# Optimization experiments

Measured on AMD Instinct MI355X. Metric: run time of the kernel, lower is better.

The kernel has to match this reference:

```python
import jax, jax.numpy as jnp
import numpy as np

B, IN, COND, H, LAT, E, GH = 8192, 256, 1024, 1024, 128, 6, 64
INP = LAT + COND      # decoder layer0 input size = 1152
INTER = LAT + H       # decoder layer1/2 input size = 1152


def setup_inputs() -> dict:
    key = jax.random.key(0)
    ks = jax.random.split(key, 30)
    n = lambda k, shape, s=0.02: jax.random.normal(k, shape, dtype=jnp.float32) * s
    return {
        'x': jax.random.normal(ks[0], (B, IN), dtype=jnp.float32),
        'y': jax.random.normal(ks[1], (B, COND), dtype=jnp.float32),
        'eps': jax.random.normal(ks[2], (B, LAT), dtype=jnp.float32),
        # encoder: layer k input = prev_dim + IN (x is re-concatenated each layer)
        'enc_w0': n(ks[3], (IN + COND + IN, H)), 'enc_b0': jnp.zeros((H,), jnp.float32),
        'enc_w1': n(ks[4], (H + IN, H)),         'enc_b1': jnp.zeros((H,), jnp.float32),
        'mu_w': n(ks[5], (H, LAT)),  'mu_b': jnp.zeros((LAT,), jnp.float32),
        'lv_w': n(ks[6], (H, LAT)),  'lv_b': jnp.zeros((LAT,), jnp.float32),
        # gating network (input = latent + cond)
        'g_w0': n(ks[7], (INP, GH)), 'g_b0': jnp.zeros((GH,), jnp.float32),
        'g_w1': n(ks[8], (GH, GH)),  'g_b1': jnp.zeros((GH,), jnp.float32),
        'g_w2': n(ks[9], (GH, E)),   'g_b2': jnp.zeros((E,), jnp.float32),
        # expert weights [E, in, out] and biases [E, out] (bias init 0.01 as in source)
        'exp_w0': n(ks[10], (E, INP, H)),   'exp_b0': jnp.full((E, H), 0.01, jnp.float32),
        'exp_w1': n(ks[11], (E, INTER, H)), 'exp_b1': jnp.full((E, H), 0.01, jnp.float32),
        'exp_w2': n(ks[12], (E, INTER, IN)), 'exp_b2': jnp.full((E, IN), 0.01, jnp.float32),
    }


def _forward(x, y, eps, enc_w0, enc_b0, enc_w1, enc_b1, mu_w, mu_b, lv_w, lv_b,
             g_w0, g_b0, g_w1, g_b1, g_w2, g_b2,
             exp_w0, exp_b0, exp_w1, exp_b1, exp_w2, exp_b2):
    elu = jax.nn.elu
    # --- Encoder ---
    h = jnp.concatenate([x, y], axis=1)
    h = elu(jnp.concatenate([h, x], axis=1) @ enc_w0 + enc_b0)
    h = elu(jnp.concatenate([h, x], axis=1) @ enc_w1 + enc_b1)
    mu = h @ mu_w + mu_b
    logvar = h @ lv_w + lv_b
    # --- Reparameterize (eps passed explicitly for determinism) ---
    z = mu + eps * jnp.exp(0.5 * logvar)
    # --- MixedDecoder ---
    g = jnp.concatenate([z, y], axis=1)
    g = elu(g @ g_w0 + g_b0)
    g = elu(g @ g_w1 + g_b1)
    coeff = jax.nn.softmax(g @ g_w2 + g_b2, axis=1)  # [B, E]
    layer_out = y
    for W, bb, act in ((exp_w0, exp_b0, True), (exp_w1, exp_b1, True), (exp_w2, exp_b2, False)):
        inp = jnp.concatenate([z, layer_out], axis=1)  # [B, I]
        # fused mixture-of-experts projection: avoids materializing per-sample [B,I,O] weight
        out = coeff @ bb + jnp.einsum('be,bi,eio->bo', coeff, inp, W)
        layer_out = elu(out) if act else out
    return layer_out, mu, logvar


def reference(x, y, eps, enc_w0, enc_b0, enc_w1, enc_b1, mu_w, mu_b, lv_w, lv_b,
              g_w0, g_b0, g_w1, g_b1, g_w2, g_b2,
              exp_w0, exp_b0, exp_w1, exp_b1, exp_w2, exp_b2):
    return _forward(x, y, eps, enc_w0, enc_b0, enc_w1, enc_b1, mu_w, mu_b, lv_w, lv_b,
                    g_w0, g_b0, g_w1, g_b1, g_w2, g_b2,
                    exp_w0, exp_b0, exp_w1, exp_b1, exp_w2, exp_b2)
```

## Files before the change

kernel.cpp:

```cpp
#include <hip/hip_runtime.h>
#include <hip/hip_bf16.h>
#include <cstddef>

using u16 = unsigned short;
using short8 = __attribute__((ext_vector_type(8))) short;
using f32x4 = __attribute__((ext_vector_type(4))) float;

constexpr int B_   = 8192;
constexpr int IN_  = 256;
constexpr int COND_= 1024;
constexpr int H_   = 1024;
constexpr int LAT_ = 128;
constexpr int NE_  = 6;
constexpr int GH_  = 64;
constexpr int INP_ = 1152;
constexpr int K0_  = 1536;
constexpr int K1_  = 1280;

constexpr int BK = 64;

typedef const __attribute__((address_space(1))) void gv_t;
typedef __attribute__((address_space(3))) void lv_t;
#define GLDS(g, l) __builtin_amdgcn_global_load_lds((gv_t*)(g), (lv_t*)(l), 16, 0, 0)

__device__ __forceinline__ u16 f2b(float f) {
  __hip_bfloat16 h = __float2bfloat16(f);
  return *reinterpret_cast<u16*>(&h);
}
__device__ __forceinline__ float elu1(float x) { return x > 0.f ? x : (__expf(x) - 1.f); }

__global__ void k_transpose(const float* __restrict__ in, u16* __restrict__ out,
                            int R, int C, long inStride, long outStride) {
  __shared__ float t[32][33];
  const float* ip = in + (long)blockIdx.z * inStride;
  u16* op = out + (long)blockIdx.z * outStride;
  int c0 = blockIdx.x * 32, r0 = blockIdx.y * 32;
  int tx = threadIdx.x, ty = threadIdx.y;
#pragma unroll
  for (int i = 0; i < 4; i++) {
    int r = r0 + ty + i * 8, c = c0 + tx;
    if (r < R && c < C) t[ty + i * 8][tx] = ip[(long)r * C + c];
  }
  __syncthreads();
#pragma unroll
  for (int i = 0; i < 4; i++) {
    int c = c0 + ty + i * 8, r = r0 + tx;
    if (r < R && c < C) op[(long)c * R + r] = f2b(t[tx][ty + i * 8]);
  }
}

__global__ void k_prep(const float* __restrict__ x, const float* __restrict__ y,
                       u16* __restrict__ A0, u16* __restrict__ A1) {
  long idx = (long)blockIdx.x * blockDim.x + threadIdx.x;
  long n0 = (long)B_ * K0_;
  if (idx < n0) {
    int b = (int)(idx / K0_), c = (int)(idx % K0_);
    float v;
    if (c < IN_)            v = x[(long)b * IN_ + c];
    else if (c < IN_+COND_) v = y[(long)b * COND_ + (c - IN_)];
    else                    v = x[(long)b * IN_ + (c - IN_ - COND_)];
    A0[idx] = f2b(v);
  } else {
    long j = idx - n0;
    if (j < (long)B_ * IN_) {
      int b = (int)(j / IN_), c = (int)(j % IN_);
      A1[(long)b * K1_ + H_ + c] = f2b(x[(long)b * IN_ + c]);
    }
  }
}

__global__ void k_z(const float* __restrict__ mu, const float* __restrict__ lv,
                    const float* __restrict__ eps, const float* __restrict__ y,
                    u16* __restrict__ ZY, u16* __restrict__ D1, u16* __restrict__ D2) {
  long idx = (long)blockIdx.x * blockDim.x + threadIdx.x;
  if (idx >= (long)B_ * INP_) return;
  int b = (int)(idx / INP_), c = (int)(idx % INP_);
  if (c < LAT_) {
    long o = (long)b * LAT_ + c;
    float z = mu[o] + eps[o] * __expf(0.5f * lv[o]);
    u16 zb = f2b(z);
    ZY[idx] = zb; D1[idx] = zb; D2[idx] = zb;
  } else {
    ZY[idx] = f2b(y[(long)b * COND_ + (c - LAT_)]);
  }
}

__global__ __launch_bounds__(256) void k_gate(const float* __restrict__ G1,
    const float* __restrict__ w1, const float* __restrict__ b1,
    const float* __restrict__ w2, const float* __restrict__ b2,
    float* __restrict__ coeff) {
  __shared__ float W1[64][65];
  __shared__ float W2[64][8];
  __shared__ float B1[64], B2[8];
  int tid = threadIdx.x;
  for (int i = tid; i < 64 * 64; i += 256) W1[i >> 6][i & 63] = w1[i];
  for (int i = tid; i < 64 * 6; i += 256) W2[i / 6][i % 6] = w2[i];
  if (tid < 64) B1[tid] = b1[tid];
  if (tid < 8)  B2[tid] = (tid < 6) ? b2[tid] : 0.f;
  __syncthreads();
  int row = blockIdx.x * 256 + tid;
  const float* gr = G1 + (long)row * GH_;
  float g[64];
#pragma unroll
  for (int i = 0; i < 16; i++) {
    float4 v = *(const float4*)(gr + i * 4);
    g[i*4] = v.x; g[i*4+1] = v.y; g[i*4+2] = v.z; g[i*4+3] = v.w;
  }
  float lg[6];
#pragma unroll
  for (int e = 0; e < 6; e++) lg[e] = B2[e];
  for (int n = 0; n < 64; n++) {
    float s = B1[n];
#pragma unroll
    for (int k = 0; k < 64; k++) s += g[k] * W1[k][n];
    s = elu1(s);
#pragma unroll
    for (int e = 0; e < 6; e++) lg[e] += s * W2[n][e];
  }
  float m = lg[0];
#pragma unroll
  for (int e = 1; e < 6; e++) m = fmaxf(m, lg[e]);
  float p[6], sum = 0.f;
#pragma unroll
  for (int e = 0; e < 6; e++) { p[e] = __expf(lg[e] - m); sum += p[e]; }
  float inv = 1.f / sum;
#pragma unroll
  for (int e = 0; e < 6; e++) coeff[(long)row * 6 + e] = p[e] * inv;
}

template<int MREP, bool MOE>
__global__ __launch_bounds__(256, 2) void k_gemm(
    const u16* __restrict__ A, int lda,
    const u16* __restrict__ WT, long wstride,
    const float* __restrict__ bias,
    const float* __restrict__ coeff,
    int N, int K, int E,
    u16* __restrict__ outH, float* __restrict__ outF, float* __restrict__ outF2,
    int ldo, int splitcol, const float* __restrict__ bias2, int act)
{
  constexpr int BMt = 32 * MREP;
  __shared__ __align__(16) u16 As[2][BMt][BK];
  __shared__ __align__(16) u16 Bs[2][128][BK];
  __shared__ float Cf[MOE ? BMt : 1][8];

  const int tid = threadIdx.x;
  const int lane = tid & 63, w = tid >> 6;
  const int wr = w >> 1, wc = w & 1;
  const int brow = blockIdx.x * BMt, bcol = blockIdx.y * 128;
  const int lr = lane & 15, hi = lane >> 4;
  const int lk = hi * 8;
  const int xsw = (lr & 7) << 3;

  if (MOE && tid < BMt) {
#pragma unroll
    for (int e2 = 0; e2 < 8; e2++)
      Cf[tid][e2] = (e2 < 6) ? coeff[(long)(brow + tid) * 6 + e2] : 0.f;
  }

  f32x4 acc[MREP][4];
#pragma unroll
  for (int m = 0; m < MREP; m++)
#pragma unroll
    for (int n = 0; n < 4; n++)
#pragma unroll
      for (int r = 0; r < 4; r++) acc[m][n][r] = 0.f;

  const int srow = w * 8 + (lane >> 3);
  const int sdst = (lane & 7) * 8;
  const int ssrc = ((lane & 7) ^ ((lane >> 3) & 7)) * 8;
  const u16* Asrc = A + (long)(brow + srow) * lda + ssrc;
  const u16* Bsrc = WT + (long)(bcol + srow) * K + ssrc;
  const int KSTEPS = K / BK;

  int cur = 0;
#pragma unroll
  for (int i = 0; i < BMt / 32; i++)
    GLDS(Asrc + (long)(i * 32) * lda, &As[0][i * 32 + srow][sdst]);
#pragma unroll
  for (int i = 0; i < 4; i++)
    GLDS(Bsrc + (long)(i * 32) * K, &Bs[0][i * 32 + srow][sdst]);

  for (int e = 0; e < E; ++e) {
    f32x4 pacc[MREP][4];
    if constexpr (MOE) {
#pragma unroll
      for (int m = 0; m < MREP; m++)
#pragma unroll
        for (int n = 0; n < 4; n++)
#pragma unroll
          for (int r = 0; r < 4; r++) pacc[m][n][r] = 0.f;
    }

    for (int kt = 0; kt < KSTEPS; ++kt) {
      __syncthreads();
      int ne = e, nk = kt + 1;
      if (nk == KSTEPS) { nk = 0; ne = e + 1; }
      if (ne < E) {
        const u16* ap = Asrc + (long)nk * BK;
        const u16* bp = Bsrc + (long)ne * wstride + (long)nk * BK;
#pragma unroll
        for (int i = 0; i < BMt / 32; i++)
          GLDS(ap + (long)(i * 32) * lda, &As[cur ^ 1][i * 32 + srow][sdst]);
#pragma unroll
        for (int i = 0; i < 4; i++)
          GLDS(bp + (long)(i * 32) * K, &Bs[cur ^ 1][i * 32 + srow][sdst]);
      }
#pragma unroll
      for (int kk = 0; kk < BK; kk += 32) {
        short8 af[MREP], bfr[4];
        const int cc = (kk + lk) ^ xsw;
#pragma unroll
        for (int m = 0; m < MREP; m++)
          af[m] = *(const short8*)&As[cur][wr * (16 * MREP) + m * 16 + lr][cc];
#pragma unroll
        for (int n = 0; n < 4; n++)
          bfr[n] = *(const short8*)&Bs[cur][wc * 64 + n * 16 + lr][cc];
#pragma unroll
        for (int m = 0; m < MREP; m++)
#pragma unroll
          for (int n = 0; n < 4; n++) {
            if constexpr (MOE)
              pacc[m][n] = __builtin_amdgcn_mfma_f32_16x16x32_bf16(af[m], bfr[n], pacc[m][n], 0, 0, 0);
            else
              acc[m][n] = __builtin_amdgcn_mfma_f32_16x16x32_bf16(af[m], bfr[n], acc[m][n], 0, 0, 0);
          }
      }
      cur ^= 1;
    }
    if constexpr (MOE) {
#pragma unroll
      for (int m = 0; m < MREP; m++)
#pragma unroll
        for (int r = 0; r < 4; r++) {
          float c = Cf[wr * (16 * MREP) + m * 16 + hi * 4 + r][e];
#pragma unroll
          for (int n = 0; n < 4; n++) acc[m][n][r] += c * pacc[m][n][r];
        }
    }
  }

#pragma unroll
  for (int m = 0; m < MREP; m++)
#pragma unroll
    for (int n = 0; n < 4; n++) {
      int col = bcol + wc * 64 + n * 16 + lr;
      if (col >= N) continue;
#pragma unroll
      for (int r = 0; r < 4; r++) {
        int rowl = wr * (16 * MREP) + m * 16 + hi * 4 + r;
        long row = brow + rowl;
        float v = acc[m][n][r];
        if constexpr (MOE) {
          float bv = 0.f;
#pragma unroll
          for (int e = 0; e < 6; e++) bv += Cf[rowl][e] * bias[(long)e * N + col];
          v += bv;
        } else {
          v += (col < splitcol) ? bias[col] : bias2[col - splitcol];
        }
        if (act) v = elu1(v);
        if (outH) outH[row * ldo + col] = f2b(v);
        else if (col < splitcol) outF[row * ldo + col] = v;
        else outF2[row * ldo + (col - splitcol)] = v;
      }
    }
}

extern "C" void kernel_launch(void* const* d_in, const int* in_sizes, int n_in,
                              void* d_out, int out_size, void* d_ws, size_t ws_size,
                              hipStream_t stream) {
  (void)in_sizes; (void)out_size;
  if (n_in < 23) return;
  const float* x      = (const float*)d_in[0];
  const float* y      = (const float*)d_in[1];
  const float* eps    = (const float*)d_in[2];
  const float* enc_w0 = (const float*)d_in[3];
  const float* enc_b0 = (const float*)d_in[4];
  const float* enc_w1 = (const float*)d_in[5];
  const float* enc_b1 = (const float*)d_in[6];
  const float* mu_w   = (const float*)d_in[7];
  const float* mu_b   = (const float*)d_in[8];
  const float* lv_w   = (const float*)d_in[9];
  const float* lv_b   = (const float*)d_in[10];
  const float* g_w0   = (const float*)d_in[11];
  const float* g_b0   = (const float*)d_in[12];
  const float* g_w1   = (const float*)d_in[13];
  const float* g_b1   = (const float*)d_in[14];
  const float* g_w2   = (const float*)d_in[15];
  const float* g_b2   = (const float*)d_in[16];
  const float* exp_w0 = (const float*)d_in[17];
  const float* exp_b0 = (const float*)d_in[18];
  const float* exp_w1 = (const float*)d_in[19];
  const float* exp_b1 = (const float*)d_in[20];
  const float* exp_w2 = (const float*)d_in[21];
  const float* exp_b2 = (const float*)d_in[22];

  char* ws = (char*)d_ws;
  size_t off = 0;
  auto alloc = [&](size_t bytes) -> void* {
    void* p = ws + off; off += (bytes + 255) & ~(size_t)255; return p;
  };
  u16* A0     = (u16*)alloc((size_t)B_ * K0_ * 2);
  u16* A1     = (u16*)alloc((size_t)B_ * K1_ * 2);
  u16* H2     = (u16*)alloc((size_t)B_ * H_ * 2);
  u16* ZY     = (u16*)alloc((size_t)B_ * INP_ * 2);
  u16* encw0T = (u16*)alloc((size_t)K0_ * H_ * 2);
  u16* encw1T = (u16*)alloc((size_t)K1_ * H_ * 2);
  u16* mulvT  = (u16*)alloc((size_t)256 * H_ * 2);
  u16* gw0T   = (u16*)alloc((size_t)GH_ * INP_ * 2);
  u16* ew0T   = (u16*)alloc((size_t)NE_ * H_ * INP_ * 2);
  if (ws_size < off) return;

  u16* D1 = A0;
  u16* D2 = A1;
  float* G1    = (float*)H2;
  float* COEFF = (float*)((char*)H2 + (size_t)B_ * GH_ * 4);
  u16* ew2T = (u16*)((char*)H2 + (size_t)4 * 1024 * 1024);
  u16* ew1T = ZY;

  float* outO = (float*)d_out;
  float* muO  = outO + (size_t)B_ * IN_;
  float* lvO  = muO + (size_t)B_ * LAT_;

  dim3 tb(32, 8);
  k_transpose<<<dim3(32, 48), tb, 0, stream>>>(enc_w0, encw0T, K0_, H_, 0, 0);
  k_transpose<<<dim3(32, 40), tb, 0, stream>>>(enc_w1, encw1T, K1_, H_, 0, 0);
  k_transpose<<<dim3(4, 32),  tb, 0, stream>>>(mu_w, mulvT, H_, LAT_, 0, 0);
  k_transpose<<<dim3(4, 32),  tb, 0, stream>>>(lv_w, mulvT + (size_t)LAT_ * H_, H_, LAT_, 0, 0);
  k_transpose<<<dim3(2, 36),  tb, 0, stream>>>(g_w0, gw0T, INP_, GH_, 0, 0);
  k_transpose<<<dim3(32, 36, NE_), tb, 0, stream>>>(exp_w0, ew0T, INP_, H_,
                                                    (long)INP_ * H_, (long)INP_ * H_);
  long npr = (long)B_ * K0_ + (long)B_ * IN_;
  k_prep<<<(int)((npr + 255) / 256), 256, 0, stream>>>(x, y, A0, A1);

  k_gemm<4, false><<<dim3(B_ / 128, H_ / 128), 256, 0, stream>>>(A0, K0_, encw0T, 0, enc_b0,
      nullptr, H_, K0_, 1, A1, nullptr, nullptr, K1_, H_, nullptr, 1);
  k_gemm<4, false><<<dim3(B_ / 128, H_ / 128), 256, 0, stream>>>(A1, K1_, encw1T, 0, enc_b1,
      nullptr, H_, K1_, 1, H2, nullptr, nullptr, H_, H_, nullptr, 1);
  k_gemm<2, false><<<dim3(B_ / 64, 2), 256, 0, stream>>>(H2, H_, mulvT, 0, mu_b, nullptr,
      256, H_, 1, nullptr, muO, lvO, LAT_, LAT_, lv_b, 0);

  k_transpose<<<dim3(8, 36, NE_), tb, 0, stream>>>(exp_w2, ew2T, INP_, IN_,
                                                   (long)INP_ * IN_, (long)INP_ * IN_);
  long nz = (long)B_ * INP_;
  k_z<<<(int)((nz + 255) / 256), 256, 0, stream>>>(muO, lvO, eps, y, ZY, D1, D2);

  k_gemm<2, false><<<dim3(B_ / 64, 1), 256, 0, stream>>>(ZY, INP_, gw0T, 0, g_b0, nullptr,
      GH_, INP_, 1, nullptr, G1, nullptr, GH_, GH_, nullptr, 1);
  k_gate<<<B_ / 256, 256, 0, stream>>>(G1, g_w1, g_b1, g_w2, g_b2, COEFF);

  k_gemm<4, true><<<dim3(B_ / 128, H_ / 128), 256, 0, stream>>>(ZY, INP_, ew0T, (long)H_ * INP_,
      exp_b0, COEFF, H_, INP_, NE_, D1 + LAT_, nullptr, nullptr, INP_, H_, nullptr, 1);
  k_transpose<<<dim3(32, 36, NE_), tb, 0, stream>>>(exp_w1, ew1T, INP_, H_,
                                                    (long)INP_ * H_, (long)INP_ * H_);
  k_gemm<4, true><<<dim3(B_ / 128, H_ / 128), 256, 0, stream>>>(D1, INP_, ew1T, (long)H_ * INP_,
      exp_b1, COEFF, H_, INP_, NE_, D2 + LAT_, nullptr, nullptr, INP_, H_, nullptr, 1);
  k_gemm<2, true><<<dim3(B_ / 64, 2), 256, 0, stream>>>(D2, INP_, ew2T, (long)IN_ * INP_,
      exp_b2, COEFF, IN_, INP_, NE_, nullptr, outO, nullptr, IN_, IN_, nullptr, 0);
}
```

Before: 599.1 us.

## Add 256x128-tile triple-buffered GEMM kernel for encoder and MoE expert layers

Introduces k_gemm8, a 512-thread kernel with 256x128 output tiles, a three-stage LDS buffer fed by global_load_lds with explicit vmcnt waits, XOR-swizzled LDS layout, and a block-index remap so blocks that share columns run close together. Both encoder GEMMs and the two large expert GEMMs now use it. The aim is more data reuse per tile and deeper overlap of loads with MFMA work. In exchange it uses more LDS and registers per block, which may lower occupancy.

```diff
diff --git a/kernel.cpp b/kernel.cpp
--- a/kernel.cpp
+++ b/kernel.cpp
@@ -126,6 +126,154 @@
   float inv = 1.f / sum;
 #pragma unroll
   for (int e = 0; e < 6; e++) coeff[(long)row * 6 + e] = p[e] * inv;
+}
+
+template<int KSTEPS, int E, bool MOE>
+__global__ __launch_bounds__(512, 2) void k_gemm8(
+    const u16* __restrict__ A,
+    const u16* __restrict__ WT,
+    const float* __restrict__ bias,
+    const float* __restrict__ coeff,
+    int N,
+    u16* __restrict__ outH, int ldo)
+{
+  constexpr int KK = KSTEPS * BK;
+  constexpr int T = E * KSTEPS;
+  __shared__ __align__(16) u16 As[3][256][BK];
+  __shared__ __align__(16) u16 Bs[3][128][BK];
+  __shared__ float Cf[MOE ? 256 : 1][8];
+
+  const int tid = threadIdx.x;
+  const int lane = tid & 63, w = tid >> 6;
+  const int wr = w >> 1, wc = w & 1;
+  const int lin = blockIdx.x + blockIdx.y * gridDim.x;
+  const int sl = (lin & 7) * 32 + (lin >> 3);
+  const int brow = (sl & 31) * 256, bcol = (sl >> 5) * 128;
+  const int lr = lane & 15, hi = lane >> 4;
+  const int lk = hi * 8;
+  const int xsw = (lr & 7) << 3;
+
+  if (MOE) {
+    if (tid < 256) {
+#pragma unroll
+      for (int e2 = 0; e2 < 8; e2++)
+        Cf[tid][e2] = (e2 < 6) ? coeff[(long)(brow + tid) * 6 + e2] : 0.f;
+    }
+    __syncthreads();
+  }
+
+  f32x4 acc[4][4];
+#pragma unroll
+  for (int m = 0; m < 4; m++)
+#pragma unroll
+    for (int n = 0; n < 4; n++)
+#pragma unroll
+      for (int r = 0; r < 4; r++) acc[m][n][r] = 0.f;
+  f32x4 pacc[MOE ? 4 : 1][MOE ? 4 : 1];
+  if constexpr (MOE) {
+#pragma unroll
+    for (int m = 0; m < 4; m++)
+#pragma unroll
+      for (int n = 0; n < 4; n++)
+#pragma unroll
+        for (int r = 0; r < 4; r++) pacc[m][n][r] = 0.f;
+  }
+
+  const int srow = w * 8 + (lane >> 3);
+  const int sdst = (lane & 7) * 8;
+  const int ssrc = ((lane & 7) ^ ((lane >> 3) & 7)) * 8;
+  const u16* Asrc = A + (long)(brow + srow) * KK + ssrc;
+  const u16* Bsrc = WT + (long)(bcol + srow) * KK + ssrc;
+
+  auto STAGE = [&](int t2, int buf) {
+    const int e2 = (E == 1) ? 0 : (t2 / KSTEPS);
+    const int k2 = (E == 1) ? t2 : (t2 % KSTEPS);
+    const u16* ap = Asrc + k2 * BK;
+    const u16* bp = Bsrc + (long)e2 * ((long)N * KK) + k2 * BK;
+#pragma unroll
+    for (int i = 0; i < 4; i++)
+      GLDS(ap + (long)(i * 64) * KK, &As[buf][i * 64 + srow][sdst]);
+#pragma unroll
+    for (int i = 0; i < 2; i++)
+      GLDS(bp + (long)(i * 64) * KK, &Bs[buf][i * 64 + srow][sdst]);
+  };
+
+  STAGE(0, 0);
+  STAGE(1, 1);
+
+  for (int t = 0; t < T; ++t) {
+    if (t + 1 < T) asm volatile("s_waitcnt vmcnt(6)" ::: "memory");
+    else           asm volatile("s_waitcnt vmcnt(0)" ::: "memory");
+    asm volatile("s_barrier" ::: "memory");
+    if (t + 2 < T) STAGE(t + 2, (t + 2) % 3);
+    const int cur = t % 3;
+#pragma unroll
+    for (int kk = 0; kk < BK; kk += 32) {
+      short8 af[4], bfr[4];
+      const int cc = (kk + lk) ^ xsw;
+#pragma unroll
+      for (int m = 0; m < 4; m++)
+        af[m] = *(const short8*)&As[cur][wr * 64 + m * 16 + lr][cc];
+#pragma unroll
+      for (int n = 0; n < 4; n++)
+        bfr[n] = *(const short8*)&Bs[cur][wc * 64 + n * 16 + lr][cc];
+      __builtin_amdgcn_s_setprio(1);
+#pragma unroll
+      for (int m = 0; m < 4; m++)
+#pragma unroll
+        for (int n = 0; n < 4; n++) {
+          if constexpr (MOE)
+            pacc[m][n] = __builtin_amdgcn_mfma_f32_16x16x32_bf16(af[m], bfr[n], pacc[m][n], 0, 0, 0);
+          else
+            acc[m][n] = __builtin_amdgcn_mfma_f32_16x16x32_bf16(af[m], bfr[n], acc[m][n], 0, 0, 0);
+        }
+      __builtin_amdgcn_s_setprio(0);
+    }
+    if constexpr (MOE) {
+      if ((t + 1) % KSTEPS == 0) {
+        const int e = t / KSTEPS;
+#pragma unroll
+        for (int m = 0; m < 4; m++)
+#pragma unroll
+          for (int r = 0; r < 4; r++) {
+            float c = Cf[wr * 64 + m * 16 + hi * 4 + r][e];
+#pragma unroll
+            for (int n = 0; n < 4; n++) acc[m][n][r] += c * pacc[m][n][r];
+          }
+        if (t + 1 < T) {
+#pragma unroll
+          for (int m = 0; m < 4; m++)
+#pragma unroll
+            for (int n = 0; n < 4; n++)
+#pragma unroll
+              for (int r = 0; r < 4; r++) pacc[m][n][r] = 0.f;
+        }
+      }
+    }
+  }
+
+#pragma unroll
+  for (int m = 0; m < 4; m++)
+#pragma unroll
+    for (int n = 0; n < 4; n++) {
+      const int col = bcol + wc * 64 + n * 16 + lr;
+#pragma unroll
+      for (int r = 0; r < 4; r++) {
+        const int rowl = wr * 64 + m * 16 + hi * 4 + r;
+        const long row = brow + rowl;
+        float v = acc[m][n][r];
+        if constexpr (MOE) {
+          float bv = 0.f;
+#pragma unroll
+          for (int e = 0; e < 6; e++) bv += Cf[rowl][e] * bias[(long)e * N + col];
+          v += bv;
+        } else {
+          v += bias[col];
+        }
+        v = elu1(v);
+        outH[row * (long)ldo + col] = f2b(v);
+      }
+    }
 }
 
 template<int MREP, bool MOE>
@@ -333,10 +481,10 @@
   long npr = (long)B_ * K0_ + (long)B_ * IN_;
   k_prep<<<(int)((npr + 255) / 256), 256, 0, stream>>>(x, y, A0, A1);
 
-  k_gemm<4, false><<<dim3(B_ / 128, H_ / 128), 256, 0, stream>>>(A0, K0_, encw0T, 0, enc_b0,
-      nullptr, H_, K0_, 1, A1, nullptr, nullptr, K1_, H_, nullptr, 1);
-  k_gemm<4, false><<<dim3(B_ / 128, H_ / 128), 256, 0, stream>>>(A1, K1_, encw1T, 0, enc_b1,
-      nullptr, H_, K1_, 1, H2, nullptr, nullptr, H_, H_, nullptr, 1);
+  k_gemm8<K0_ / BK, 1, false><<<dim3(32, 8), 512, 0, stream>>>(A0, encw0T, enc_b0,
+      nullptr, H_, A1, K1_);
+  k_gemm8<K1_ / BK, 1, false><<<dim3(32, 8), 512, 0, stream>>>(A1, encw1T, enc_b1,
+      nullptr, H_, H2, H_);
   k_gemm<2, false><<<dim3(B_ / 64, 2), 256, 0, stream>>>(H2, H_, mulvT, 0, mu_b, nullptr,
       256, H_, 1, nullptr, muO, lvO, LAT_, LAT_, lv_b, 0);
 
@@ -349,12 +497,12 @@
       GH_, INP_, 1, nullptr, G1, nullptr, GH_, GH_, nullptr, 1);
   k_gate<<<B_ / 256, 256, 0, stream>>>(G1, g_w1, g_b1, g_w2, g_b2, COEFF);
 
-  k_gemm<4, true><<<dim3(B_ / 128, H_ / 128), 256, 0, stream>>>(ZY, INP_, ew0T, (long)H_ * INP_,
-      exp_b0, COEFF, H_, INP_, NE_, D1 + LAT_, nullptr, nullptr, INP_, H_, nullptr, 1);
+  k_gemm8<INP_ / BK, NE_, true><<<dim3(32, 8), 512, 0, stream>>>(ZY, ew0T, exp_b0,
+      COEFF, H_, D1 + LAT_, INP_);
   k_transpose<<<dim3(32, 36, NE_), tb, 0, stream>>>(exp_w1, ew1T, INP_, H_,
                                                     (long)INP_ * H_, (long)INP_ * H_);
-  k_gemm<4, true><<<dim3(B_ / 128, H_ / 128), 256, 0, stream>>>(D1, INP_, ew1T, (long)H_ * INP_,
-      exp_b1, COEFF, H_, INP_, NE_, D2 + LAT_, nullptr, nullptr, INP_, H_, nullptr, 1);
+  k_gemm8<INP_ / BK, NE_, true><<<dim3(32, 8), 512, 0, stream>>>(D1, ew1T, exp_b1,
+      COEFF, H_, D2 + LAT_, INP_);
   k_gemm<2, true><<<dim3(B_ / 64, 2), 256, 0, stream>>>(D2, INP_, ew2T, (long)IN_ * INP_,
       exp_b2, COEFF, IN_, INP_, NE_, nullptr, outO, nullptr, IN_, IN_, nullptr, 0);
 }
```

Result: slower. 666.7 us (+11.3%).
